# Performance work log

Hardware: AMD Instinct MI355X
Metric: run time of the kernel (lower is better)

## Reference

```python
import jax, jax.numpy as jnp
import numpy as np

EPS_IN = 1e-5  # torch InstanceNorm2d default eps

def _gather(a, idx):
    # a: [B,C,N], idx: [B,M,K] -> [B,C,M,K]
    return jax.vmap(lambda ab, ib: ab[:, ib])(a, idx)

def _inorm(v, w, b):
    # InstanceNorm2d over spatial dims (M,K), per batch per channel, affine
    mean = v.mean(axis=(2, 3), keepdims=True)
    var = v.var(axis=(2, 3), keepdims=True)
    return (v - mean) * jax.lax.rsqrt(var + EPS_IN) * w[None, :, None, None] + b[None, :, None, None]

def setup_inputs() -> dict:
    key = jax.random.key(0)
    ks = jax.random.split(key, 10)
    B, N, M, K = 4, 8192, 8192, 16
    Cin, Cout, KS, DIM = 64, 64, 16, 3
    inp = {
        'x': jax.random.normal(ks[0], (B, Cin, N), dtype=jnp.float32),
        'pos': jax.random.normal(ks[1], (B, DIM, N), dtype=jnp.float32),
        'support_points': jax.random.normal(ks[2], (B, DIM, M), dtype=jnp.float32),
        'neighbors_indices': jax.random.randint(ks[3], (B, M, K), 0, N, dtype=jnp.int32),
        'alpha': jnp.ones((1,), jnp.float32),
        'beta': jnp.ones((1,), jnp.float32),
        'norm_radius': jnp.ones((1,), jnp.float32),
        'fc1_w': jax.random.normal(ks[4], (KS, DIM), jnp.float32) * 0.3,
        'fc2_w': jax.random.normal(ks[5], (KS, 2 * KS), jnp.float32) * 0.15,
        'fc3_w': jax.random.normal(ks[6], (KS, 2 * KS), jnp.float32) * 0.15,
        'bn1_w': jnp.ones((KS,), jnp.float32), 'bn1_b': jnp.zeros((KS,), jnp.float32),
        'bn2_w': jnp.ones((KS,), jnp.float32), 'bn2_b': jnp.zeros((KS,), jnp.float32),
        'cv_w': jax.random.normal(ks[7], (Cout, Cin, KS), jnp.float32) * (1.0 / np.sqrt(Cin * KS)),
    }
    return inp

def reference(x, pos, support_points, neighbors_indices, alpha, beta, norm_radius,
              fc1_w, fc2_w, fc3_w, bn1_w, bn1_b, bn2_w, bn2_b, cv_w):
    # eval mode, adaptive_normalization=True, K>1 branch (K=16)
    pos_g = _gather(pos, neighbors_indices)            # [B,3,M,K]
    x_g = _gather(x, neighbors_indices)                # [B,Cin,M,K]
    pts = pos_g - support_points[:, :, :, None]        # [B,3,M,K]
    K = pts.shape[3]

    # distances computed on detached pts in torch
    d = jnp.sqrt((jax.lax.stop_gradient(pts) ** 2).sum(axis=1))  # [B,M,K]
    pts = pts / norm_radius
    dw = jax.nn.sigmoid(-alpha * d + beta)             # [B,M,K]
    dws = dw.sum(axis=2, keepdims=True)
    dws = dws + (dws == 0).astype(dw.dtype) + 1e-6
    dw = (dw / dws * K)[:, None]                       # [B,1,M,K]

    mat = jax.nn.relu(_inorm(jnp.einsum('oc,bcmk->bomk', fc1_w, pts), bn1_w, bn1_b))  # [B,16,M,K]
    mp1 = jnp.max(mat * dw, axis=3, keepdims=True)
    mat = jnp.concatenate([mat, jnp.broadcast_to(mp1, mat.shape)], axis=1)            # [B,32,M,K]
    mat = jax.nn.relu(_inorm(jnp.einsum('oc,bcmk->bomk', fc2_w, mat), bn2_w, bn2_b))
    mp2 = jnp.max(mat * dw, axis=3, keepdims=True)
    mat = jnp.concatenate([mat, jnp.broadcast_to(mp2, mat.shape)], axis=1)
    mat = jax.nn.relu(jnp.einsum('oc,bcmk->bomk', fc3_w, mat)) * dw                   # [B,16,M,K]

    # features = x_g^T @ mat over K, then 1x16 conv contracting the 16-kernel axis
    feat = jnp.einsum('bcmk,bjmk->bcmj', x_g, mat)     # [B,Cin,M,16]
    out = jnp.einsum('ocj,bcmj->bom', cv_w, feat)      # [B,Cout,M]
    return out
```

## Files before the change

kernel.cpp:

```cpp
#include <hip/hip_runtime.h>
#include <math.h>

#define BB 4
#define NN 8192
#define MM 8192
#define KK 16

#define WS_CVB_BYTE  2048
#define WS_XT_BYTE   (WS_CVB_BYTE + 131072)
#define WS_PT_BYTE   (WS_XT_BYTE + 4194304)
#define WS_MOMP_BYTE (WS_PT_BYTE + 524288)
#define WS_P2_BYTE   (WS_MOMP_BYTE + 6144)
#define WS_SB_BYTE   (WS_P2_BYTE + 65536)

#define OV_STRIDE 1040
#define M3_STRIDE 384

typedef __bf16 bhalf;
typedef bhalf bhalf8 __attribute__((ext_vector_type(8)));
typedef float f32x4 __attribute__((ext_vector_type(4)));
typedef ushort ushort8v __attribute__((ext_vector_type(8)));
typedef ushort ushort4v __attribute__((ext_vector_type(4)));

static __device__ __forceinline__ ushort f2b(float f) {
    return __builtin_bit_cast(ushort, (__bf16)f);
}

template <int CTRL>
__device__ __forceinline__ float dpp_rot(float v) {
    int r = __builtin_amdgcn_update_dpp(0, __builtin_bit_cast(int, v), CTRL, 0xF, 0xF, true);
    return __builtin_bit_cast(float, r);
}
__device__ __forceinline__ float gmax16(float v) {
    v = fmaxf(v, dpp_rot<0x121>(v));
    v = fmaxf(v, dpp_rot<0x122>(v));
    v = fmaxf(v, dpp_rot<0x124>(v));
    v = fmaxf(v, dpp_rot<0x128>(v));
    return v;
}
__device__ __forceinline__ float gsum16(float v) {
    v += dpp_rot<0x121>(v);
    v += dpp_rot<0x122>(v);
    v += dpp_rot<0x124>(v);
    v += dpp_rot<0x128>(v);
    return v;
}

__global__ __launch_bounds__(256) void k_pre(const float* __restrict__ x,
                                             const float* __restrict__ pos,
                                             const float* __restrict__ sup,
                                             const int* __restrict__ nbr,
                                             const float* __restrict__ cv,
                                             float* __restrict__ momp,
                                             ushort* __restrict__ cvb,
                                             ushort* __restrict__ xT,
                                             float* __restrict__ posT) {
    int bid = blockIdx.x, t = threadIdx.x;
    if (bid < 512) {
        int b = bid >> 7, n0 = (bid & 127) * 64;
        __shared__ ushort tile[64 * 66];
        const float* xb = x + (size_t)b * 64 * NN;
#pragma unroll
        for (int i = 0; i < 16; i++) {
            int c = i * 4 + (t >> 6), n = t & 63;
            tile[c * 66 + n] = f2b(xb[(size_t)c * NN + n0 + n]);
        }
        __syncthreads();
#pragma unroll
        for (int i = 0; i < 16; i++) {
            int n = i * 4 + (t >> 6), c = t & 63;
            xT[((size_t)b * NN + n0 + n) * 64 + c] = tile[c * 66 + n];
        }
        int nl = t >> 2, d = t & 3;
        float v = (d < 3) ? pos[((size_t)b * 3 + d) * NN + n0 + nl] : 0.f;
        posT[((size_t)b * NN + n0 + nl) * 4 + d] = v;
    } else if (bid < 576) {
        int e = (bid - 512) * 1024 + t * 4;
        float4 cvv = *(const float4*)(cv + e);
        ushort4v o = {f2b(cvv.x), f2b(cvv.y), f2b(cvv.z), f2b(cvv.w)};
        *(ushort4v*)(cvb + e) = o;
    } else {
        __shared__ float redm[36];
        int rem = bid - 576;
        int b = rem & 3, m = (rem >> 2) * 256 + t;
        const float* posb = pos + (size_t)b * 3 * NN;
        float sx = sup[((size_t)b * 3 + 0) * MM + m];
        float sy = sup[((size_t)b * 3 + 1) * MM + m];
        float sz = sup[((size_t)b * 3 + 2) * MM + m];
        const int* nb = nbr + ((size_t)b * MM + m) * KK;
        float s[9] = {0, 0, 0, 0, 0, 0, 0, 0, 0};
#pragma unroll
        for (int k = 0; k < KK; k++) {
            int id = nb[k];
            float px = posb[id] - sx, py = posb[NN + id] - sy, pz = posb[2 * NN + id] - sz;
            s[0] += px; s[1] += py; s[2] += pz;
            s[3] += px * px; s[4] += py * py; s[5] += pz * pz;
            s[6] += px * py; s[7] += px * pz; s[8] += py * pz;
        }
#pragma unroll
        for (int i = 0; i < 9; i++) {
            float v = s[i];
#pragma unroll
            for (int off = 32; off >= 1; off >>= 1) v += __shfl_down(v, off);
            if ((t & 63) == 0) redm[(t >> 6) * 9 + i] = v;
        }
        __syncthreads();
        if (t < 9) momp[rem * 12 + t] = redm[t] + redm[9 + t] + redm[18 + t] + redm[27 + t];
    }
}

__global__ __launch_bounds__(256) void k_stats2(const float* __restrict__ sup,
                                                const int* __restrict__ nbr,
                                                const float* __restrict__ alpha_,
                                                const float* __restrict__ beta_,
                                                const float* __restrict__ nr_,
                                                const float* __restrict__ fc1,
                                                const float* __restrict__ fc2,
                                                const float* __restrict__ bn1w,
                                                const float* __restrict__ bn1b,
                                                const float* __restrict__ posT,
                                                const float* __restrict__ momp,
                                                float* __restrict__ p2) {
    __shared__ float sc1[16], bi1[16], momr[9], red[4 * 33];
    int t = threadIdx.x, b = blockIdx.y;
    if (t < 9) {
        float s = 0.f;
#pragma unroll
        for (int g = 0; g < 32; g++) s += momp[(4 * g + b) * 12 + t];
        momr[t] = s;
    }
    __syncthreads();
    if (t < 16) {
        float inv = 1.f / (float)(MM * KK);
        float inr = 1.f / nr_[0];
        float mux = momr[0] * inv * inr, muy = momr[1] * inv * inr, muz = momr[2] * inv * inr;
        float i2 = inv * inr * inr;
        float w0 = fc1[t * 3], w1v = fc1[t * 3 + 1], w2v = fc1[t * 3 + 2];
        float mean = w0 * mux + w1v * muy + w2v * muz;
        float ey2 = w0 * w0 * momr[3] * i2 + w1v * w1v * momr[4] * i2 + w2v * w2v * momr[5] * i2 +
                    2.f * (w0 * w1v * momr[6] * i2 + w0 * w2v * momr[7] * i2 + w1v * w2v * momr[8] * i2);
        float var = fmaxf(ey2 - mean * mean, 0.f);
        float rs = rsqrtf(var + 1e-5f);
        sc1[t] = bn1w[t] * rs;
        bi1[t] = bn1b[t] - mean * sc1[t];
    }
    __syncthreads();
    int mi = t >> 2, kq = t & 3;
    int m = blockIdx.x * 64 + mi;
    float alpha = alpha_[0], beta = beta_[0], inr = 1.f / nr_[0];
    float sx = sup[((size_t)b * 3 + 0) * MM + m];
    float sy = sup[((size_t)b * 3 + 1) * MM + m];
    float sz = sup[((size_t)b * 3 + 2) * MM + m];
    const int* nb = nbr + ((size_t)b * MM + m) * KK + kq * 4;

    float q1m[16], G1[16], G2[16];
#pragma unroll
    for (int j = 0; j < 16; j++) { q1m[j] = 0.f; G1[j] = 0.f; G2[j] = 0.f; }
    float S = 0.f;
#pragma unroll
    for (int kk = 0; kk < 4; kk++) {
        int id = nb[kk];
        float4 pv = *(const float4*)(posT + ((size_t)b * NN + id) * 4);
        float rx = pv.x - sx, ry = pv.y - sy, rz = pv.z - sz;
        float dd = sqrtf(rx * rx + ry * ry + rz * rz);
        float srk = 1.f / (1.f + expf(alpha * dd - beta));
        S += srk;
        float nxv = rx * inr, nyv = ry * inr, nzv = rz * inr;
        float m1c[16];
#pragma unroll
        for (int j = 0; j < 16; j++) {
            float y = fc1[j * 3] * nxv + fc1[j * 3 + 1] * nyv + fc1[j * 3 + 2] * nzv;
            m1c[j] = fmaxf(y * sc1[j] + bi1[j], 0.f);
            q1m[j] = fmaxf(q1m[j], m1c[j] * srk);
        }
#pragma unroll
        for (int c = 0; c < 16; c++) {
            float g = 0.f;
#pragma unroll
            for (int q = 0; q < 4; q++) {
                float4 v = *(const float4*)(fc2 + c * 32 + q * 4);
                g += v.x * m1c[q * 4] + v.y * m1c[q * 4 + 1] +
                     v.z * m1c[q * 4 + 2] + v.w * m1c[q * 4 + 3];
            }
            G1[c] += g; G2[c] += g * g;
        }
    }
    S += __shfl_xor(S, 1); S += __shfl_xor(S, 2);
#pragma unroll
    for (int j = 0; j < 16; j++) {
        q1m[j] = fmaxf(q1m[j], __shfl_xor(q1m[j], 1));
        q1m[j] = fmaxf(q1m[j], __shfl_xor(q1m[j], 2));
    }
    S = S + (S == 0.f ? 1.f : 0.f) + 1e-6f;
    float fac = 16.f / S;
#pragma unroll
    for (int c = 0; c < 16; c++) {
        float h2 = 0.f;
#pragma unroll
        for (int q = 0; q < 4; q++) {
            float4 v = *(const float4*)(fc2 + c * 32 + 16 + q * 4);
            h2 += v.x * q1m[q * 4] + v.y * q1m[q * 4 + 1] +
                  v.z * q1m[q * 4 + 2] + v.w * q1m[q * 4 + 3];
        }
        h2 *= fac;
        float s2p = G1[c] + 4.f * h2;
        float q2p = G2[c] + 2.f * h2 * G1[c] + 4.f * h2 * h2;
#pragma unroll
        for (int off = 32; off >= 1; off >>= 1) {
            s2p += __shfl_down(s2p, off);
            q2p += __shfl_down(q2p, off);
        }
        if ((t & 63) == 0) {
            red[(t >> 6) * 33 + c] = s2p;
            red[(t >> 6) * 33 + 16 + c] = q2p;
        }
    }
    __syncthreads();
    if (t < 32)
        p2[((size_t)b * 128 + blockIdx.x) * 32 + t] =
            red[t] + red[33 + t] + red[66 + t] + red[99 + t];
}

__global__ __launch_bounds__(256) void k_fin(const float* __restrict__ momp,
                                             const float* __restrict__ p2,
                                             const float* __restrict__ fc1,
                                             const float* __restrict__ bn1w,
                                             const float* __restrict__ bn1b,
                                             const float* __restrict__ bn2w,
                                             const float* __restrict__ bn2b,
                                             const float* __restrict__ nr_,
                                             float* __restrict__ sb) {
    __shared__ float red[8 * 33], momr[9];
    int b = blockIdx.x, t = threadIdx.x;
    int c = t & 31, ch = t >> 5;
    float s = 0.f;
#pragma unroll
    for (int g = 0; g < 16; g++) s += p2[((size_t)b * 128 + ch * 16 + g) * 32 + c];
    red[ch * 33 + c] = s;
    if (t < 9) {
        float v = 0.f;
#pragma unroll
        for (int g = 0; g < 32; g++) v += momp[(4 * g + b) * 12 + t];
        momr[t] = v;
    }
    __syncthreads();
    if (t < 16) {
        float inv = 1.f / (float)(MM * KK);
        float inr = 1.f / nr_[0];
        float mux = momr[0] * inv * inr, muy = momr[1] * inv * inr, muz = momr[2] * inv * inr;
        float i2 = inv * inr * inr;
        float w0 = fc1[t * 3], wa = fc1[t * 3 + 1], wb = fc1[t * 3 + 2];
        float mean = w0 * mux + wa * muy + wb * muz;
        float ey2 = w0 * w0 * momr[3] * i2 + wa * wa * momr[4] * i2 + wb * wb * momr[5] * i2 +
                    2.f * (w0 * wa * momr[6] * i2 + w0 * wb * momr[7] * i2 + wa * wb * momr[8] * i2);
        float var = fmaxf(ey2 - mean * mean, 0.f);
        float rs = rsqrtf(var + 1e-5f);
        float s1v = bn1w[t] * rs;
        float b1v = bn1b[t] - mean * s1v;
        float sum2 = 0.f, ssq2 = 0.f;
#pragma unroll
        for (int chh = 0; chh < 8; chh++) {
            sum2 += red[chh * 33 + t];
            ssq2 += red[chh * 33 + 16 + t];
        }
        float mean2 = sum2 * inv;
        float var2 = fmaxf(ssq2 * inv - mean2 * mean2, 0.f);
        float rs2 = rsqrtf(var2 + 1e-5f);
        float s2v = bn2w[t] * rs2;
        float b2v = bn2b[t] - mean2 * s2v;
        sb[b * 64 + t] = s1v;
        sb[b * 64 + 16 + t] = b1v;
        sb[b * 64 + 32 + t] = s2v;
        sb[b * 64 + 48 + t] = b2v;
    }
}

__global__ __launch_bounds__(256, 3) void k_final(const float* __restrict__ sup,
                                               const int* __restrict__ nbr,
                                               const float* __restrict__ alpha_,
                                               const float* __restrict__ beta_,
                                               const float* __restrict__ nr_,
                                               const float* __restrict__ fc1,
                                               const float* __restrict__ fc2,
                                               const float* __restrict__ fc3,
                                               const float* __restrict__ sb,
                                               const ushort* __restrict__ cvb,
                                               const ushort* __restrict__ xT,
                                               const float* __restrict__ posT,
                                               float* __restrict__ out) {
    __shared__ __align__(16) ushort ov[16 * OV_STRIDE];
    __shared__ __align__(16) ushort m3l[16 * M3_STRIDE];

    int t = threadIdx.x;
    int b = blockIdx.y;
    int m0 = blockIdx.x * 16;
    int w = t >> 6, l = t & 63;
    int lk = l & 15, kg = l >> 4;
    int ps = t >> 4, ks = t & 15;

    int idxt = nbr[((size_t)b * MM + m0 + ps) * KK + ks];
    float4 pf = *(const float4*)(posT + ((size_t)b * NN + idxt) * 4);
    const ushort8v* xrow = (const ushort8v*)(xT + ((size_t)b * NN + idxt) * 64);
    ushort8v g0 = xrow[0], g1 = xrow[1], g2 = xrow[2], g3 = xrow[3];
    ushort8v g4 = xrow[4], g5 = xrow[5], g6 = xrow[6], g7 = xrow[7];
    float4 w2b0 = *(const float4*)(fc2 + ks * 32 + 16);
    float4 w2b1 = *(const float4*)(fc2 + ks * 32 + 20);
    float4 w2b2 = *(const float4*)(fc2 + ks * 32 + 24);
    float4 w2b3 = *(const float4*)(fc2 + ks * 32 + 28);
    float4 w3b0 = *(const float4*)(fc3 + ks * 32 + 16);
    float4 w3b1 = *(const float4*)(fc3 + ks * 32 + 20);
    float4 w3b2 = *(const float4*)(fc3 + ks * 32 + 24);
    float4 w3b3 = *(const float4*)(fc3 + ks * 32 + 28);

    float alpha = alpha_[0], beta = beta_[0], inr = 1.f / nr_[0];
    const float* sbb = sb + b * 64;

    {
        int mm = m0 + ps;
        float rx = pf.x - sup[((size_t)b * 3 + 0) * MM + mm];
        float ry = pf.y - sup[((size_t)b * 3 + 1) * MM + mm];
        float rz = pf.z - sup[((size_t)b * 3 + 2) * MM + mm];
        float dd = sqrtf(rx * rx + ry * ry + rz * rz);
        float sr = 1.f / (1.f + expf(alpha * dd - beta));
        float S = gsum16(sr);
        S = S + (S == 0.f ? 1.f : 0.f) + 1e-6f;
        float dwk = sr * (16.f / S);
        float nxv = rx * inr, nyv = ry * inr, nzv = rz * inr;

        float m1v[16], mp1[16];
#pragma unroll
        for (int j = 0; j < 16; j++) {
            float y = fc1[j * 3] * nxv + fc1[j * 3 + 1] * nyv + fc1[j * 3 + 2] * nzv;
            m1v[j] = fmaxf(y * sbb[j] + sbb[16 + j], 0.f);
        }
#pragma unroll
        for (int j = 0; j < 16; j++) mp1[j] = gmax16(m1v[j] * dwk);

        float h2own = w2b0.x * mp1[0] + w2b0.y * mp1[1] + w2b0.z * mp1[2] + w2b0.w * mp1[3]
                    + w2b1.x * mp1[4] + w2b1.y * mp1[5] + w2b1.z * mp1[6] + w2b1.w * mp1[7]
                    + w2b2.x * mp1[8] + w2b2.y * mp1[9] + w2b2.z * mp1[10] + w2b2.w * mp1[11]
                    + w2b3.x * mp1[12] + w2b3.y * mp1[13] + w2b3.z * mp1[14] + w2b3.w * mp1[15];
        int pbase = l & 48;
        float m2v[16], mp2[16];
#pragma unroll
        for (int c = 0; c < 16; c++) {
            float a = 0.f;
#pragma unroll
            for (int q = 0; q < 4; q++) {
                float4 v = *(const float4*)(fc2 + c * 32 + q * 4);
                a += v.x * m1v[q * 4] + v.y * m1v[q * 4 + 1] + v.z * m1v[q * 4 + 2] + v.w * m1v[q * 4 + 3];
            }
            a += __shfl(h2own, pbase + c);
            m2v[c] = fmaxf(a * sbb[32 + c] + sbb[48 + c], 0.f);
        }
#pragma unroll
        for (int c = 0; c < 16; c++) mp2[c] = gmax16(m2v[c] * dwk);

        float h3own = w3b0.x * mp2[0] + w3b0.y * mp2[1] + w3b0.z * mp2[2] + w3b0.w * mp2[3]
                    + w3b1.x * mp2[4] + w3b1.y * mp2[5] + w3b1.z * mp2[6] + w3b1.w * mp2[7]
                    + w3b2.x * mp2[8] + w3b2.y * mp2[9] + w3b2.z * mp2[10] + w3b2.w * mp2[11]
                    + w3b3.x * mp2[12] + w3b3.y * mp2[13] + w3b3.z * mp2[14] + w3b3.w * mp2[15];
        ushort* m3p = m3l + ps * M3_STRIDE;
#pragma unroll
        for (int j = 0; j < 16; j++) {
            float a = 0.f;
#pragma unroll
            for (int q = 0; q < 4; q++) {
                float4 v = *(const float4*)(fc3 + j * 32 + q * 4);
                a += v.x * m2v[q * 4] + v.y * m2v[q * 4 + 1] + v.z * m2v[q * 4 + 2] + v.w * m2v[q * 4 + 3];
            }
            a += __shfl(h3own, pbase + j);
            m3p[j * 24 + ks] = f2b(fmaxf(a, 0.f) * dwk);
        }
    }

    {
        ushort* ovp = ov + ps * OV_STRIDE;
#define STG(gv, h) _Pragma("unroll") for (int i2 = 0; i2 < 8; i2++) ovp[((h) * 8 + i2) * 16 + ks] = (ushort)gv[i2];
        STG(g0, 0) STG(g1, 1) STG(g2, 2) STG(g3, 3)
        STG(g4, 4) STG(g5, 5) STG(g6, 6) STG(g7, 7)
#undef STG
    }

    const f32x4 zz = {0.f, 0.f, 0.f, 0.f};

#pragma unroll
    for (int pp = 0; pp < 4; pp++) {
        int p = w * 4 + pp;
        bhalf8 afr = {};
        if (kg < 2) afr = __builtin_bit_cast(bhalf8, *(ushort8v*)(m3l + p * M3_STRIDE + lk * 24 + kg * 8));
        ushort* ovb = ov + p * OV_STRIDE;
#pragma unroll
        for (int cb = 0; cb < 4; cb++) {
            bhalf8 bfr = {};
            if (kg < 2) bfr = __builtin_bit_cast(bhalf8, *(ushort8v*)(ovb + (cb * 16 + lk) * 16 + kg * 8));
            f32x4 dF = __builtin_amdgcn_mfma_f32_16x16x32_bf16(afr, bfr, zz, 0, 0, 0);
            ushort4v fw = {f2b(dF[0]), f2b(dF[1]), f2b(dF[2]), f2b(dF[3])};
            *(ushort4v*)(ovb + (cb * 16 + lk) * 16 + kg * 4) = fw;
        }
    }

    const ushort* arow = cvb + (size_t)(w * 16 + lk) * 1024;
    ushort8v aupre0 = *(const ushort8v*)(arow + 0 * 32 + kg * 8);
    ushort8v aupre1 = *(const ushort8v*)(arow + 1 * 32 + kg * 8);
    ushort8v aupre2 = *(const ushort8v*)(arow + 2 * 32 + kg * 8);
    ushort8v aupre3 = *(const ushort8v*)(arow + 3 * 32 + kg * 8);

    __syncthreads();

    {
        const ushort* brow = ov + lk * OV_STRIDE;
        f32x4 acc0 = zz, acc1 = zz;
#pragma unroll
        for (int kt = 0; kt < 32; kt += 2) {
            bhalf8 au0, au1;
            if (kt == 0) {
                au0 = __builtin_bit_cast(bhalf8, aupre0);
                au1 = __builtin_bit_cast(bhalf8, aupre1);
            } else if (kt == 2) {
                au0 = __builtin_bit_cast(bhalf8, aupre2);
                au1 = __builtin_bit_cast(bhalf8, aupre3);
            } else {
                au0 = __builtin_bit_cast(bhalf8, *(const ushort8v*)(arow + kt * 32 + kg * 8));
                au1 = __builtin_bit_cast(bhalf8, *(const ushort8v*)(arow + (kt + 1) * 32 + kg * 8));
            }
            bhalf8 bu0 = __builtin_bit_cast(bhalf8, *(const ushort8v*)(brow + kt * 32 + kg * 8));
            bhalf8 bu1 = __builtin_bit_cast(bhalf8, *(const ushort8v*)(brow + (kt + 1) * 32 + kg * 8));
            acc0 = __builtin_amdgcn_mfma_f32_16x16x32_bf16(au0, bu0, acc0, 0, 0, 0);
            acc1 = __builtin_amdgcn_mfma_f32_16x16x32_bf16(au1, bu1, acc1, 0, 0, 0);
        }
#pragma unroll
        for (int r = 0; r < 4; r++) {
            int o = w * 16 + kg * 4 + r;
            out[((size_t)(b * 64 + o)) * MM + m0 + lk] = acc0[r] + acc1[r];
        }
    }
}

extern "C" void kernel_launch(void* const* d_in, const int* in_sizes, int n_in,
                              void* d_out, int out_size, void* d_ws, size_t ws_size,
                              hipStream_t stream) {
    const float* x    = (const float*)d_in[0];
    const float* pos  = (const float*)d_in[1];
    const float* sup  = (const float*)d_in[2];
    const int*   nbr  = (const int*)d_in[3];
    const float* alp  = (const float*)d_in[4];
    const float* bet  = (const float*)d_in[5];
    const float* nr   = (const float*)d_in[6];
    const float* fc1  = (const float*)d_in[7];
    const float* fc2  = (const float*)d_in[8];
    const float* fc3  = (const float*)d_in[9];
    const float* bn1w = (const float*)d_in[10];
    const float* bn1b = (const float*)d_in[11];
    const float* bn2w = (const float*)d_in[12];
    const float* bn2b = (const float*)d_in[13];
    const float* cv   = (const float*)d_in[14];
    float* out = (float*)d_out;
    ushort* cvb  = (ushort*)((char*)d_ws + WS_CVB_BYTE);
    ushort* xT   = (ushort*)((char*)d_ws + WS_XT_BYTE);
    float*  posT = (float*)((char*)d_ws + WS_PT_BYTE);
    float*  momp = (float*)((char*)d_ws + WS_MOMP_BYTE);
    float*  p2   = (float*)((char*)d_ws + WS_P2_BYTE);
    float*  sb   = (float*)((char*)d_ws + WS_SB_BYTE);

    k_pre<<<704, 256, 0, stream>>>(x, pos, sup, nbr, cv, momp, cvb, xT, posT);
    k_stats2<<<dim3(128, BB), 256, 0, stream>>>(sup, nbr, alp, bet, nr, fc1, fc2,
                                                bn1w, bn1b, posT, momp, p2);
    k_fin<<<BB, 256, 0, stream>>>(momp, p2, fc1, bn1w, bn1b, bn2w, bn2b, nr, sb);
    k_final<<<dim3(512, BB), 256, 0, stream>>>(sup, nbr, alp, bet, nr, fc1, fc2, fc3,
                                               sb, cvb, xT, posT, out);
}
```

Measured before the change: 89.76 us.

## Split final kernel into mat3 MLP kernel and gather-GEMM kernel via global buffer

The fused final kernel is split in two. k_mat3 computes the per-neighbor MLP weights and writes them as bf16 to a workspace buffer (B*M*256 values). k_gemm gathers the x rows, loads those weights straight from global memory into MFMA fragments, and does the feature and conv contractions. The aim is lower register and LDS pressure per kernel so more waves fit on a CU (launch bounds 5 and 4 instead of 3). In exchange it adds an extra launch, a 16 MB write and read-back of the intermediate, and a second read of nbr.

```diff
diff --git a/kernel.cpp b/kernel.cpp
--- a/kernel.cpp
+++ b/kernel.cpp
@@ -12,9 +12,9 @@
 #define WS_MOMP_BYTE (WS_PT_BYTE + 524288)
 #define WS_P2_BYTE   (WS_MOMP_BYTE + 6144)
 #define WS_SB_BYTE   (WS_P2_BYTE + 65536)
+#define WS_M3_BYTE   (WS_SB_BYTE + 1024)
 
 #define OV_STRIDE 1040
-#define M3_STRIDE 384
 
 typedef __bf16 bhalf;
 typedef bhalf bhalf8 __attribute__((ext_vector_type(8)));
@@ -275,34 +275,26 @@
     }
 }
 
-__global__ __launch_bounds__(256, 3) void k_final(const float* __restrict__ sup,
-                                               const int* __restrict__ nbr,
-                                               const float* __restrict__ alpha_,
-                                               const float* __restrict__ beta_,
-                                               const float* __restrict__ nr_,
-                                               const float* __restrict__ fc1,
-                                               const float* __restrict__ fc2,
-                                               const float* __restrict__ fc3,
-                                               const float* __restrict__ sb,
-                                               const ushort* __restrict__ cvb,
-                                               const ushort* __restrict__ xT,
-                                               const float* __restrict__ posT,
-                                               float* __restrict__ out) {
-    __shared__ __align__(16) ushort ov[16 * OV_STRIDE];
-    __shared__ __align__(16) ushort m3l[16 * M3_STRIDE];
-
+__global__ __launch_bounds__(256, 5) void k_mat3(const float* __restrict__ sup,
+                                                 const int* __restrict__ nbr,
+                                                 const float* __restrict__ alpha_,
+                                                 const float* __restrict__ beta_,
+                                                 const float* __restrict__ nr_,
+                                                 const float* __restrict__ fc1,
+                                                 const float* __restrict__ fc2,
+                                                 const float* __restrict__ fc3,
+                                                 const float* __restrict__ sb,
+                                                 const float* __restrict__ posT,
+                                                 ushort* __restrict__ m3g) {
     int t = threadIdx.x;
     int b = blockIdx.y;
     int m0 = blockIdx.x * 16;
-    int w = t >> 6, l = t & 63;
-    int lk = l & 15, kg = l >> 4;
+    int l = t & 63;
     int ps = t >> 4, ks = t & 15;
-
-    int idxt = nbr[((size_t)b * MM + m0 + ps) * KK + ks];
+    int mm = m0 + ps;
+
+    int idxt = nbr[((size_t)b * MM + mm) * KK + ks];
     float4 pf = *(const float4*)(posT + ((size_t)b * NN + idxt) * 4);
-    const ushort8v* xrow = (const ushort8v*)(xT + ((size_t)b * NN + idxt) * 64);
-    ushort8v g0 = xrow[0], g1 = xrow[1], g2 = xrow[2], g3 = xrow[3];
-    ushort8v g4 = xrow[4], g5 = xrow[5], g6 = xrow[6], g7 = xrow[7];
     float4 w2b0 = *(const float4*)(fc2 + ks * 32 + 16);
     float4 w2b1 = *(const float4*)(fc2 + ks * 32 + 20);
     float4 w2b2 = *(const float4*)(fc2 + ks * 32 + 24);
@@ -315,63 +307,90 @@
     float alpha = alpha_[0], beta = beta_[0], inr = 1.f / nr_[0];
     const float* sbb = sb + b * 64;
 
-    {
-        int mm = m0 + ps;
-        float rx = pf.x - sup[((size_t)b * 3 + 0) * MM + mm];
-        float ry = pf.y - sup[((size_t)b * 3 + 1) * MM + mm];
-        float rz = pf.z - sup[((size_t)b * 3 + 2) * MM + mm];
-        float dd = sqrtf(rx * rx + ry * ry + rz * rz);
-        float sr = 1.f / (1.f + expf(alpha * dd - beta));
-        float S = gsum16(sr);
-        S = S + (S == 0.f ? 1.f : 0.f) + 1e-6f;
-        float dwk = sr * (16.f / S);
-        float nxv = rx * inr, nyv = ry * inr, nzv = rz * inr;
-
-        float m1v[16], mp1[16];
-#pragma unroll
-        for (int j = 0; j < 16; j++) {
-            float y = fc1[j * 3] * nxv + fc1[j * 3 + 1] * nyv + fc1[j * 3 + 2] * nzv;
-            m1v[j] = fmaxf(y * sbb[j] + sbb[16 + j], 0.f);
-        }
-#pragma unroll
-        for (int j = 0; j < 16; j++) mp1[j] = gmax16(m1v[j] * dwk);
-
-        float h2own = w2b0.x * mp1[0] + w2b0.y * mp1[1] + w2b0.z * mp1[2] + w2b0.w * mp1[3]
-                    + w2b1.x * mp1[4] + w2b1.y * mp1[5] + w2b1.z * mp1[6] + w2b1.w * mp1[7]
-                    + w2b2.x * mp1[8] + w2b2.y * mp1[9] + w2b2.z * mp1[10] + w2b2.w * mp1[11]
-                    + w2b3.x * mp1[12] + w2b3.y * mp1[13] + w2b3.z * mp1[14] + w2b3.w * mp1[15];
-        int pbase = l & 48;
-        float m2v[16], mp2[16];
-#pragma unroll
-        for (int c = 0; c < 16; c++) {
-            float a = 0.f;
-#pragma unroll
-            for (int q = 0; q < 4; q++) {
-                float4 v = *(const float4*)(fc2 + c * 32 + q * 4);
-                a += v.x * m1v[q * 4] + v.y * m1v[q * 4 + 1] + v.z * m1v[q * 4 + 2] + v.w * m1v[q * 4 + 3];
-            }
-            a += __shfl(h2own, pbase + c);
-            m2v[c] = fmaxf(a * sbb[32 + c] + sbb[48 + c], 0.f);
-        }
-#pragma unroll
-        for (int c = 0; c < 16; c++) mp2[c] = gmax16(m2v[c] * dwk);
-
-        float h3own = w3b0.x * mp2[0] + w3b0.y * mp2[1] + w3b0.z * mp2[2] + w3b0.w * mp2[3]
-                    + w3b1.x * mp2[4] + w3b1.y * mp2[5] + w3b1.z * mp2[6] + w3b1.w * mp2[7]
-                    + w3b2.x * mp2[8] + w3b2.y * mp2[9] + w3b2.z * mp2[10] + w3b2.w * mp2[11]
-                    + w3b3.x * mp2[12] + w3b3.y * mp2[13] + w3b3.z * mp2[14] + w3b3.w * mp2[15];
-        ushort* m3p = m3l + ps * M3_STRIDE;
-#pragma unroll
-        for (int j = 0; j < 16; j++) {
-            float a = 0.f;
-#pragma unroll
-            for (int q = 0; q < 4; q++) {
-                float4 v = *(const float4*)(fc3 + j * 32 + q * 4);
-                a += v.x * m2v[q * 4] + v.y * m2v[q * 4 + 1] + v.z * m2v[q * 4 + 2] + v.w * m2v[q * 4 + 3];
-            }
-            a += __shfl(h3own, pbase + j);
-            m3p[j * 24 + ks] = f2b(fmaxf(a, 0.f) * dwk);
-        }
+    float rx = pf.x - sup[((size_t)b * 3 + 0) * MM + mm];
+    float ry = pf.y - sup[((size_t)b * 3 + 1) * MM + mm];
+    float rz = pf.z - sup[((size_t)b * 3 + 2) * MM + mm];
+    float dd = sqrtf(rx * rx + ry * ry + rz * rz);
+    float sr = 1.f / (1.f + expf(alpha * dd - beta));
+    float S = gsum16(sr);
+    S = S + (S == 0.f ? 1.f : 0.f) + 1e-6f;
+    float dwk = sr * (16.f / S);
+    float nxv = rx * inr, nyv = ry * inr, nzv = rz * inr;
+
+    float m1v[16], mp1[16];
+#pragma unroll
+    for (int j = 0; j < 16; j++) {
+        float y = fc1[j * 3] * nxv + fc1[j * 3 + 1] * nyv + fc1[j * 3 + 2] * nzv;
+        m1v[j] = fmaxf(y * sbb[j] + sbb[16 + j], 0.f);
+    }
+#pragma unroll
+    for (int j = 0; j < 16; j++) mp1[j] = gmax16(m1v[j] * dwk);
+
+    float h2own = w2b0.x * mp1[0] + w2b0.y * mp1[1] + w2b0.z * mp1[2] + w2b0.w * mp1[3]
+                + w2b1.x * mp1[4] + w2b1.y * mp1[5] + w2b1.z * mp1[6] + w2b1.w * mp1[7]
+                + w2b2.x * mp1[8] + w2b2.y * mp1[9] + w2b2.z * mp1[10] + w2b2.w * mp1[11]
+                + w2b3.x * mp1[12] + w2b3.y * mp1[13] + w2b3.z * mp1[14] + w2b3.w * mp1[15];
+    int pbase = l & 48;
+    float m2v[16], mp2[16];
+#pragma unroll
+    for (int c = 0; c < 16; c++) {
+        float a = 0.f;
+#pragma unroll
+        for (int q = 0; q < 4; q++) {
+            float4 v = *(const float4*)(fc2 + c * 32 + q * 4);
+            a += v.x * m1v[q * 4] + v.y * m1v[q * 4 + 1] + v.z * m1v[q * 4 + 2] + v.w * m1v[q * 4 + 3];
+        }
+        a += __shfl(h2own, pbase + c);
+        m2v[c] = fmaxf(a * sbb[32 + c] + sbb[48 + c], 0.f);
+    }
+#pragma unroll
+    for (int c = 0; c < 16; c++) mp2[c] = gmax16(m2v[c] * dwk);
+
+    float h3own = w3b0.x * mp2[0] + w3b0.y * mp2[1] + w3b0.z * mp2[2] + w3b0.w * mp2[3]
+                + w3b1.x * mp2[4] + w3b1.y * mp2[5] + w3b1.z * mp2[6] + w3b1.w * mp2[7]
+                + w3b2.x * mp2[8] + w3b2.y * mp2[9] + w3b2.z * mp2[10] + w3b2.w * mp2[11]
+                + w3b3.x * mp2[12] + w3b3.y * mp2[13] + w3b3.z * mp2[14] + w3b3.w * mp2[15];
+    ushort* m3p = m3g + ((size_t)b * MM + mm) * 256;
+#pragma unroll
+    for (int j = 0; j < 16; j++) {
+        float a = 0.f;
+#pragma unroll
+        for (int q = 0; q < 4; q++) {
+            float4 v = *(const float4*)(fc3 + j * 32 + q * 4);
+            a += v.x * m2v[q * 4] + v.y * m2v[q * 4 + 1] + v.z * m2v[q * 4 + 2] + v.w * m2v[q * 4 + 3];
+        }
+        a += __shfl(h3own, pbase + j);
+        m3p[j * 16 + ks] = f2b(fmaxf(a, 0.f) * dwk);
+    }
+}
+
+__global__ __launch_bounds__(256, 4) void k_gemm(const int* __restrict__ nbr,
+                                                 const ushort* __restrict__ m3g,
+                                                 const ushort* __restrict__ cvb,
+                                                 const ushort* __restrict__ xT,
+                                                 float* __restrict__ out) {
+    __shared__ __align__(16) ushort ov[16 * OV_STRIDE];
+
+    int t = threadIdx.x;
+    int b = blockIdx.y;
+    int m0 = blockIdx.x * 16;
+    int w = t >> 6, l = t & 63;
+    int lk = l & 15, kg = l >> 4;
+    int ps = t >> 4, ks = t & 15;
+
+    int idxt = nbr[((size_t)b * MM + m0 + ps) * KK + ks];
+    const ushort8v* xrow = (const ushort8v*)(xT + ((size_t)b * NN + idxt) * 64);
+    ushort8v g0 = xrow[0], g1 = xrow[1], g2 = xrow[2], g3 = xrow[3];
+    ushort8v g4 = xrow[4], g5 = xrow[5], g6 = xrow[6], g7 = xrow[7];
+
+    ushort8v afrp[4];
+#pragma unroll
+    for (int pp = 0; pp < 4; pp++) {
+        int p = w * 4 + pp;
+        if (kg < 2)
+            afrp[pp] = *(const ushort8v*)(m3g + ((size_t)b * MM + m0 + p) * 256 + lk * 16 + kg * 8);
+        else
+            afrp[pp] = (ushort8v){0, 0, 0, 0, 0, 0, 0, 0};
     }
 
     {
@@ -387,8 +406,7 @@
 #pragma unroll
     for (int pp = 0; pp < 4; pp++) {
         int p = w * 4 + pp;
-        bhalf8 afr = {};
-        if (kg < 2) afr = __builtin_bit_cast(bhalf8, *(ushort8v*)(m3l + p * M3_STRIDE + lk * 24 + kg * 8));
+        bhalf8 afr = __builtin_bit_cast(bhalf8, afrp[pp]);
         ushort* ovb = ov + p * OV_STRIDE;
 #pragma unroll
         for (int cb = 0; cb < 4; cb++) {
@@ -462,11 +480,13 @@
     float*  momp = (float*)((char*)d_ws + WS_MOMP_BYTE);
     float*  p2   = (float*)((char*)d_ws + WS_P2_BYTE);
     float*  sb   = (float*)((char*)d_ws + WS_SB_BYTE);
+    ushort* m3g  = (ushort*)((char*)d_ws + WS_M3_BYTE);
 
     k_pre<<<704, 256, 0, stream>>>(x, pos, sup, nbr, cv, momp, cvb, xT, posT);
     k_stats2<<<dim3(128, BB), 256, 0, stream>>>(sup, nbr, alp, bet, nr, fc1, fc2,
                                                 bn1w, bn1b, posT, momp, p2);
     k_fin<<<BB, 256, 0, stream>>>(momp, p2, fc1, bn1w, bn1b, bn2w, bn2b, nr, sb);
-    k_final<<<dim3(512, BB), 256, 0, stream>>>(sup, nbr, alp, bet, nr, fc1, fc2, fc3,
-                                               sb, cvb, xT, posT, out);
-}
+    k_mat3<<<dim3(512, BB), 256, 0, stream>>>(sup, nbr, alp, bet, nr, fc1, fc2, fc3,
+                                              sb, posT, m3g);
+    k_gemm<<<dim3(512, BB), 256, 0, stream>>>(nbr, m3g, cvb, xT, out);
+}
```

After: 101.1 us, median of 2. +12.6%, slower.

## Process four M-tiles per block with software-prefetched neighbor gathers

Applied to the files above, without the earlier changes.

Each block of k_final now handles four consecutive 16-point tiles in a loop instead of one. The gather of the next tile's neighbor indices, positions, x rows and support coordinates is issued before the current tile's MFMA stages, so the loads can overlap with compute. The cv weight preloads are also amortized across tiles. The LDS row stride changes from 1040 to 1032. In exchange the grid shrinks to a quarter, each tile adds two barriers, and the carried prefetch registers increase register pressure at the 3-block launch bound.

```diff
diff --git a/kernel.cpp b/kernel.cpp
--- a/kernel.cpp
+++ b/kernel.cpp
@@ -13,8 +13,9 @@
 #define WS_P2_BYTE   (WS_MOMP_BYTE + 6144)
 #define WS_SB_BYTE   (WS_P2_BYTE + 65536)
 
-#define OV_STRIDE 1040
+#define OV_STRIDE 1032
 #define M3_STRIDE 384
+#define TPB 4
 
 typedef __bf16 bhalf;
 typedef bhalf bhalf8 __attribute__((ext_vector_type(8)));
@@ -293,16 +294,11 @@
 
     int t = threadIdx.x;
     int b = blockIdx.y;
-    int m0 = blockIdx.x * 16;
+    int base = blockIdx.x * (16 * TPB);
     int w = t >> 6, l = t & 63;
     int lk = l & 15, kg = l >> 4;
     int ps = t >> 4, ks = t & 15;
 
-    int idxt = nbr[((size_t)b * MM + m0 + ps) * KK + ks];
-    float4 pf = *(const float4*)(posT + ((size_t)b * NN + idxt) * 4);
-    const ushort8v* xrow = (const ushort8v*)(xT + ((size_t)b * NN + idxt) * 64);
-    ushort8v g0 = xrow[0], g1 = xrow[1], g2 = xrow[2], g3 = xrow[3];
-    ushort8v g4 = xrow[4], g5 = xrow[5], g6 = xrow[6], g7 = xrow[7];
     float4 w2b0 = *(const float4*)(fc2 + ks * 32 + 16);
     float4 w2b1 = *(const float4*)(fc2 + ks * 32 + 20);
     float4 w2b2 = *(const float4*)(fc2 + ks * 32 + 24);
@@ -311,128 +307,149 @@
     float4 w3b1 = *(const float4*)(fc3 + ks * 32 + 20);
     float4 w3b2 = *(const float4*)(fc3 + ks * 32 + 24);
     float4 w3b3 = *(const float4*)(fc3 + ks * 32 + 28);
-
-    float alpha = alpha_[0], beta = beta_[0], inr = 1.f / nr_[0];
-    const float* sbb = sb + b * 64;
-
-    {
-        int mm = m0 + ps;
-        float rx = pf.x - sup[((size_t)b * 3 + 0) * MM + mm];
-        float ry = pf.y - sup[((size_t)b * 3 + 1) * MM + mm];
-        float rz = pf.z - sup[((size_t)b * 3 + 2) * MM + mm];
-        float dd = sqrtf(rx * rx + ry * ry + rz * rz);
-        float sr = 1.f / (1.f + expf(alpha * dd - beta));
-        float S = gsum16(sr);
-        S = S + (S == 0.f ? 1.f : 0.f) + 1e-6f;
-        float dwk = sr * (16.f / S);
-        float nxv = rx * inr, nyv = ry * inr, nzv = rz * inr;
-
-        float m1v[16], mp1[16];
-#pragma unroll
-        for (int j = 0; j < 16; j++) {
-            float y = fc1[j * 3] * nxv + fc1[j * 3 + 1] * nyv + fc1[j * 3 + 2] * nzv;
-            m1v[j] = fmaxf(y * sbb[j] + sbb[16 + j], 0.f);
-        }
-#pragma unroll
-        for (int j = 0; j < 16; j++) mp1[j] = gmax16(m1v[j] * dwk);
-
-        float h2own = w2b0.x * mp1[0] + w2b0.y * mp1[1] + w2b0.z * mp1[2] + w2b0.w * mp1[3]
-                    + w2b1.x * mp1[4] + w2b1.y * mp1[5] + w2b1.z * mp1[6] + w2b1.w * mp1[7]
-                    + w2b2.x * mp1[8] + w2b2.y * mp1[9] + w2b2.z * mp1[10] + w2b2.w * mp1[11]
-                    + w2b3.x * mp1[12] + w2b3.y * mp1[13] + w2b3.z * mp1[14] + w2b3.w * mp1[15];
-        int pbase = l & 48;
-        float m2v[16], mp2[16];
-#pragma unroll
-        for (int c = 0; c < 16; c++) {
-            float a = 0.f;
-#pragma unroll
-            for (int q = 0; q < 4; q++) {
-                float4 v = *(const float4*)(fc2 + c * 32 + q * 4);
-                a += v.x * m1v[q * 4] + v.y * m1v[q * 4 + 1] + v.z * m1v[q * 4 + 2] + v.w * m1v[q * 4 + 3];
-            }
-            a += __shfl(h2own, pbase + c);
-            m2v[c] = fmaxf(a * sbb[32 + c] + sbb[48 + c], 0.f);
-        }
-#pragma unroll
-        for (int c = 0; c < 16; c++) mp2[c] = gmax16(m2v[c] * dwk);
-
-        float h3own = w3b0.x * mp2[0] + w3b0.y * mp2[1] + w3b0.z * mp2[2] + w3b0.w * mp2[3]
-                    + w3b1.x * mp2[4] + w3b1.y * mp2[5] + w3b1.z * mp2[6] + w3b1.w * mp2[7]
-                    + w3b2.x * mp2[8] + w3b2.y * mp2[9] + w3b2.z * mp2[10] + w3b2.w * mp2[11]
-                    + w3b3.x * mp2[12] + w3b3.y * mp2[13] + w3b3.z * mp2[14] + w3b3.w * mp2[15];
-        ushort* m3p = m3l + ps * M3_STRIDE;
-#pragma unroll
-        for (int j = 0; j < 16; j++) {
-            float a = 0.f;
-#pragma unroll
-            for (int q = 0; q < 4; q++) {
-                float4 v = *(const float4*)(fc3 + j * 32 + q * 4);
-                a += v.x * m2v[q * 4] + v.y * m2v[q * 4 + 1] + v.z * m2v[q * 4 + 2] + v.w * m2v[q * 4 + 3];
-            }
-            a += __shfl(h3own, pbase + j);
-            m3p[j * 24 + ks] = f2b(fmaxf(a, 0.f) * dwk);
-        }
-    }
-
-    {
-        ushort* ovp = ov + ps * OV_STRIDE;
-#define STG(gv, h) _Pragma("unroll") for (int i2 = 0; i2 < 8; i2++) ovp[((h) * 8 + i2) * 16 + ks] = (ushort)gv[i2];
-        STG(g0, 0) STG(g1, 1) STG(g2, 2) STG(g3, 3)
-        STG(g4, 4) STG(g5, 5) STG(g6, 6) STG(g7, 7)
-#undef STG
-    }
-
-    const f32x4 zz = {0.f, 0.f, 0.f, 0.f};
-
-#pragma unroll
-    for (int pp = 0; pp < 4; pp++) {
-        int p = w * 4 + pp;
-        bhalf8 afr = {};
-        if (kg < 2) afr = __builtin_bit_cast(bhalf8, *(ushort8v*)(m3l + p * M3_STRIDE + lk * 24 + kg * 8));
-        ushort* ovb = ov + p * OV_STRIDE;
-#pragma unroll
-        for (int cb = 0; cb < 4; cb++) {
-            bhalf8 bfr = {};
-            if (kg < 2) bfr = __builtin_bit_cast(bhalf8, *(ushort8v*)(ovb + (cb * 16 + lk) * 16 + kg * 8));
-            f32x4 dF = __builtin_amdgcn_mfma_f32_16x16x32_bf16(afr, bfr, zz, 0, 0, 0);
-            ushort4v fw = {f2b(dF[0]), f2b(dF[1]), f2b(dF[2]), f2b(dF[3])};
-            *(ushort4v*)(ovb + (cb * 16 + lk) * 16 + kg * 4) = fw;
-        }
-    }
-
     const ushort* arow = cvb + (size_t)(w * 16 + lk) * 1024;
     ushort8v aupre0 = *(const ushort8v*)(arow + 0 * 32 + kg * 8);
     ushort8v aupre1 = *(const ushort8v*)(arow + 1 * 32 + kg * 8);
     ushort8v aupre2 = *(const ushort8v*)(arow + 2 * 32 + kg * 8);
     ushort8v aupre3 = *(const ushort8v*)(arow + 3 * 32 + kg * 8);
 
-    __syncthreads();
-
-    {
-        const ushort* brow = ov + lk * OV_STRIDE;
-        f32x4 acc0 = zz, acc1 = zz;
-#pragma unroll
-        for (int kt = 0; kt < 32; kt += 2) {
-            bhalf8 au0, au1;
-            if (kt == 0) {
-                au0 = __builtin_bit_cast(bhalf8, aupre0);
-                au1 = __builtin_bit_cast(bhalf8, aupre1);
-            } else if (kt == 2) {
-                au0 = __builtin_bit_cast(bhalf8, aupre2);
-                au1 = __builtin_bit_cast(bhalf8, aupre3);
-            } else {
-                au0 = __builtin_bit_cast(bhalf8, *(const ushort8v*)(arow + kt * 32 + kg * 8));
-                au1 = __builtin_bit_cast(bhalf8, *(const ushort8v*)(arow + (kt + 1) * 32 + kg * 8));
-            }
-            bhalf8 bu0 = __builtin_bit_cast(bhalf8, *(const ushort8v*)(brow + kt * 32 + kg * 8));
-            bhalf8 bu1 = __builtin_bit_cast(bhalf8, *(const ushort8v*)(brow + (kt + 1) * 32 + kg * 8));
-            acc0 = __builtin_amdgcn_mfma_f32_16x16x32_bf16(au0, bu0, acc0, 0, 0, 0);
-            acc1 = __builtin_amdgcn_mfma_f32_16x16x32_bf16(au1, bu1, acc1, 0, 0, 0);
-        }
-#pragma unroll
-        for (int r = 0; r < 4; r++) {
-            int o = w * 16 + kg * 4 + r;
-            out[((size_t)(b * 64 + o)) * MM + m0 + lk] = acc0[r] + acc1[r];
+    float alpha = alpha_[0], beta = beta_[0], inr = 1.f / nr_[0];
+    const float* sbb = sb + b * 64;
+    const f32x4 zz = {0.f, 0.f, 0.f, 0.f};
+
+    int idxc = nbr[((size_t)b * MM + base + ps) * KK + ks];
+    float4 pf = *(const float4*)(posT + ((size_t)b * NN + idxc) * 4);
+    const ushort8v* xr = (const ushort8v*)(xT + ((size_t)b * NN + idxc) * 64);
+    ushort8v g0 = xr[0], g1 = xr[1], g2 = xr[2], g3 = xr[3];
+    ushort8v g4 = xr[4], g5 = xr[5], g6 = xr[6], g7 = xr[7];
+    float sxr = sup[((size_t)b * 3 + 0) * MM + base + ps];
+    float syr = sup[((size_t)b * 3 + 1) * MM + base + ps];
+    float szr = sup[((size_t)b * 3 + 2) * MM + base + ps];
+
+#pragma unroll
+    for (int mt = 0; mt < TPB; ++mt) {
+        int m0 = base + mt * 16;
+        int nmt = (mt + 1 < TPB) ? (mt + 1) : (TPB - 1);
+        int idxn = nbr[((size_t)b * MM + base + nmt * 16 + ps) * KK + ks];
+
+        {
+            float rx = pf.x - sxr, ry = pf.y - syr, rz = pf.z - szr;
+            float dd = sqrtf(rx * rx + ry * ry + rz * rz);
+            float sr = 1.f / (1.f + expf(alpha * dd - beta));
+            float S = gsum16(sr);
+            S = S + (S == 0.f ? 1.f : 0.f) + 1e-6f;
+            float dwk = sr * (16.f / S);
+            float nxv = rx * inr, nyv = ry * inr, nzv = rz * inr;
+
+            float m1v[16], mp1[16];
+#pragma unroll
+            for (int j = 0; j < 16; j++) {
+                float y = fc1[j * 3] * nxv + fc1[j * 3 + 1] * nyv + fc1[j * 3 + 2] * nzv;
+                m1v[j] = fmaxf(y * sbb[j] + sbb[16 + j], 0.f);
+            }
+#pragma unroll
+            for (int j = 0; j < 16; j++) mp1[j] = gmax16(m1v[j] * dwk);
+
+            float h2own = w2b0.x * mp1[0] + w2b0.y * mp1[1] + w2b0.z * mp1[2] + w2b0.w * mp1[3]
+                        + w2b1.x * mp1[4] + w2b1.y * mp1[5] + w2b1.z * mp1[6] + w2b1.w * mp1[7]
+                        + w2b2.x * mp1[8] + w2b2.y * mp1[9] + w2b2.z * mp1[10] + w2b2.w * mp1[11]
+                        + w2b3.x * mp1[12] + w2b3.y * mp1[13] + w2b3.z * mp1[14] + w2b3.w * mp1[15];
+            int pbase = l & 48;
+            float m2v[16], mp2[16];
+#pragma unroll
+            for (int c = 0; c < 16; c++) {
+                float a = 0.f;
+#pragma unroll
+                for (int q = 0; q < 4; q++) {
+                    float4 v = *(const float4*)(fc2 + c * 32 + q * 4);
+                    a += v.x * m1v[q * 4] + v.y * m1v[q * 4 + 1] + v.z * m1v[q * 4 + 2] + v.w * m1v[q * 4 + 3];
+                }
+                a += __shfl(h2own, pbase + c);
+                m2v[c] = fmaxf(a * sbb[32 + c] + sbb[48 + c], 0.f);
+            }
+#pragma unroll
+            for (int c = 0; c < 16; c++) mp2[c] = gmax16(m2v[c] * dwk);
+
+            float h3own = w3b0.x * mp2[0] + w3b0.y * mp2[1] + w3b0.z * mp2[2] + w3b0.w * mp2[3]
+                        + w3b1.x * mp2[4] + w3b1.y * mp2[5] + w3b1.z * mp2[6] + w3b1.w * mp2[7]
+                        + w3b2.x * mp2[8] + w3b2.y * mp2[9] + w3b2.z * mp2[10] + w3b2.w * mp2[11]
+                        + w3b3.x * mp2[12] + w3b3.y * mp2[13] + w3b3.z * mp2[14] + w3b3.w * mp2[15];
+            ushort* m3p = m3l + ps * M3_STRIDE;
+#pragma unroll
+            for (int j = 0; j < 16; j++) {
+                float a = 0.f;
+#pragma unroll
+                for (int q = 0; q < 4; q++) {
+                    float4 v = *(const float4*)(fc3 + j * 32 + q * 4);
+                    a += v.x * m2v[q * 4] + v.y * m2v[q * 4 + 1] + v.z * m2v[q * 4 + 2] + v.w * m2v[q * 4 + 3];
+                }
+                a += __shfl(h3own, pbase + j);
+                m3p[j * 24 + ks] = f2b(fmaxf(a, 0.f) * dwk);
+            }
+        }
+
+        __syncthreads();
+
+        {
+            ushort* ovp = ov + ps * OV_STRIDE;
+#define STG(gv, h) _Pragma("unroll") for (int i2 = 0; i2 < 8; i2++) ovp[((h) * 8 + i2) * 16 + ks] = (ushort)gv[i2];
+            STG(g0, 0) STG(g1, 1) STG(g2, 2) STG(g3, 3)
+            STG(g4, 4) STG(g5, 5) STG(g6, 6) STG(g7, 7)
+#undef STG
+        }
+
+        pf = *(const float4*)(posT + ((size_t)b * NN + idxn) * 4);
+        xr = (const ushort8v*)(xT + ((size_t)b * NN + idxn) * 64);
+        g0 = xr[0]; g1 = xr[1]; g2 = xr[2]; g3 = xr[3];
+        g4 = xr[4]; g5 = xr[5]; g6 = xr[6]; g7 = xr[7];
+        sxr = sup[((size_t)b * 3 + 0) * MM + base + nmt * 16 + ps];
+        syr = sup[((size_t)b * 3 + 1) * MM + base + nmt * 16 + ps];
+        szr = sup[((size_t)b * 3 + 2) * MM + base + nmt * 16 + ps];
+
+#pragma unroll
+        for (int pp = 0; pp < 4; pp++) {
+            int p = w * 4 + pp;
+            bhalf8 afr = {};
+            if (kg < 2) afr = __builtin_bit_cast(bhalf8, *(ushort8v*)(m3l + p * M3_STRIDE + lk * 24 + kg * 8));
+            ushort* ovb = ov + p * OV_STRIDE;
+#pragma unroll
+            for (int cb = 0; cb < 4; cb++) {
+                bhalf8 bfr = {};
+                if (kg < 2) bfr = __builtin_bit_cast(bhalf8, *(ushort8v*)(ovb + (cb * 16 + lk) * 16 + kg * 8));
+                f32x4 dF = __builtin_amdgcn_mfma_f32_16x16x32_bf16(afr, bfr, zz, 0, 0, 0);
+                ushort4v fw = {f2b(dF[0]), f2b(dF[1]), f2b(dF[2]), f2b(dF[3])};
+                *(ushort4v*)(ovb + (cb * 16 + lk) * 16 + kg * 4) = fw;
+            }
+        }
+
+        __syncthreads();
+
+        {
+            const ushort* brow = ov + lk * OV_STRIDE;
+            f32x4 acc0 = zz, acc1 = zz;
+#pragma unroll
+            for (int kt = 0; kt < 32; kt += 2) {
+                bhalf8 au0, au1;
+                if (kt == 0) {
+                    au0 = __builtin_bit_cast(bhalf8, aupre0);
+                    au1 = __builtin_bit_cast(bhalf8, aupre1);
+                } else if (kt == 2) {
+                    au0 = __builtin_bit_cast(bhalf8, aupre2);
+                    au1 = __builtin_bit_cast(bhalf8, aupre3);
+                } else {
+                    au0 = __builtin_bit_cast(bhalf8, *(const ushort8v*)(arow + kt * 32 + kg * 8));
+                    au1 = __builtin_bit_cast(bhalf8, *(const ushort8v*)(arow + (kt + 1) * 32 + kg * 8));
+                }
+                bhalf8 bu0 = __builtin_bit_cast(bhalf8, *(const ushort8v*)(brow + kt * 32 + kg * 8));
+                bhalf8 bu1 = __builtin_bit_cast(bhalf8, *(const ushort8v*)(brow + (kt + 1) * 32 + kg * 8));
+                acc0 = __builtin_amdgcn_mfma_f32_16x16x32_bf16(au0, bu0, acc0, 0, 0, 0);
+                acc1 = __builtin_amdgcn_mfma_f32_16x16x32_bf16(au1, bu1, acc1, 0, 0, 0);
+            }
+#pragma unroll
+            for (int r = 0; r < 4; r++) {
+                int o = w * 16 + kg * 4 + r;
+                out[((size_t)(b * 64 + o)) * MM + m0 + lk] = acc0[r] + acc1[r];
+            }
         }
     }
 }
@@ -467,6 +484,7 @@
     k_stats2<<<dim3(128, BB), 256, 0, stream>>>(sup, nbr, alp, bet, nr, fc1, fc2,
                                                 bn1w, bn1b, posT, momp, p2);
     k_fin<<<BB, 256, 0, stream>>>(momp, p2, fc1, bn1w, bn1b, bn2w, bn2b, nr, sb);
-    k_final<<<dim3(512, BB), 256, 0, stream>>>(sup, nbr, alp, bet, nr, fc1, fc2, fc3,
-                                               sb, cvb, xT, posT, out);
-}
+    k_final<<<dim3(MM / (16 * TPB), BB), 256, 0, stream>>>(sup, nbr, alp, bet, nr,
+                                                           fc1, fc2, fc3, sb, cvb,
+                                                           xT, posT, out);
+}
```

New measurement: 96.82 us. 7.9% more time.
